# Kernel tuning notes

Measured on AMD Instinct MI355X. Metric: run time of the kernel, lower is better.

Reference implementation:

```python
import jax, jax.numpy as jnp
import numpy as np

EPS = 1e-6
NHEAD = 12

def _ln(x):
    m = jnp.mean(x, -1, keepdims=True)
    v = jnp.var(x, -1, keepdims=True)
    return (x - m) * jax.lax.rsqrt(v + EPS)

def _modulate(x, shift, scale):
    return x * (1 + scale[:, None, :]) + shift[:, None, :]

def _pos_embedding(idx, dim, max_len=2048):
    K = jnp.arange(dim // 2)
    ang = idx[..., None] * jnp.pi / (max_len ** (2.0 * K / dim))
    return jnp.concatenate([jnp.sin(ang), jnp.cos(ang)], axis=-1)

def _forward(x, W_xemb, b_xemb, ds_table, sg_table, Wqkv, bqkv, Wo, bo, W1, b1, W2, b2,
             Wada, bada, Wada_f, bada_f, W_out, dataset, spacegroup, mask):
    B, N, _ = x.shape
    D = W_xemb.shape[1]
    hd = D // NHEAD
    # conditioning vector: label embeddings (eval mode: no cfg dropout)
    c = ds_table[dataset] + sg_table[spacegroup]                 # [B, D]
    h = x @ W_xemb + b_xemb + _pos_embedding(jnp.arange(N), D)[None]  # [B, N, D]
    kmask = mask[:, None, None, :]                                # [B,1,1,N], True = padded key
    scale_qk = 1.0 / jnp.sqrt(jnp.asarray(hd, h.dtype))

    def block(h, p):
        Wqkv, bqkv, Wo, bo, W1, b1, W2, b2, Wada, bada = p
        mods = jax.nn.silu(c) @ Wada + bada                      # [B, 6D]
        sh_a, sc_a, g_a, sh_m, sc_m, g_m = jnp.split(mods, 6, axis=-1)
        xm = _modulate(_ln(h), sh_a, sc_a)
        qkv = (xm @ Wqkv + bqkv).reshape(B, N, 3, NHEAD, hd)
        q, k, v = qkv[:, :, 0], qkv[:, :, 1], qkv[:, :, 2]
        scores = jnp.einsum('bqhd,bkhd->bhqk', q, k) * scale_qk   # MATH-backend path: full [B,H,N,N]
        scores = jnp.where(kmask, -jnp.inf, scores)
        attn = jax.nn.softmax(scores, axis=-1)
        o = jnp.einsum('bhqk,bkhd->bqhd', attn, v).reshape(B, N, D)
        o = o @ Wo + bo
        h = h + g_a[:, None, :] * o
        y = _modulate(_ln(h), sh_m, sc_m)
        y = jax.nn.gelu(y @ W1 + b1, approximate=True) @ W2 + b2
        h = h + g_m[:, None, :] * y
        return h, None

    h, _ = jax.lax.scan(block, h, (Wqkv, bqkv, Wo, bo, W1, b1, W2, b2, Wada, bada))
    mods_f = jax.nn.silu(c) @ Wada_f + bada_f
    sh_f, sc_f = jnp.split(mods_f, 2, axis=-1)
    return _modulate(_ln(h), sh_f, sc_f) @ W_out                  # [B, N, 1] per-token energy


def setup_inputs() -> dict:
    B, N, D, L, DX, HID = 32, 512, 768, 12, 8, 3072
    keys = iter(jax.random.split(jax.random.key(0), 32))
    def w(shape, s=0.02):
        return jax.random.normal(next(keys), shape, jnp.float32) * s
    return dict(
        x=jax.random.normal(next(keys), (B, N, 2 * DX), jnp.float32),
        W_xemb=w((2 * DX, D)), b_xemb=jnp.zeros((D,), jnp.float32),
        ds_table=w((3, D)), sg_table=w((231, D)),
        Wqkv=w((L, D, 3 * D)), bqkv=jnp.zeros((L, 3 * D), jnp.float32),
        Wo=w((L, D, D)), bo=jnp.zeros((L, D), jnp.float32),
        W1=w((L, D, HID)), b1=jnp.zeros((L, HID), jnp.float32),
        W2=w((L, HID, D)), b2=jnp.zeros((L, D), jnp.float32),
        Wada=w((L, D, 6 * D)), bada=jnp.zeros((L, 6 * D), jnp.float32),
        Wada_f=w((D, 2 * D)), bada_f=jnp.zeros((2 * D,), jnp.float32),
        W_out=w((D, 1)),
        dataset=jax.random.randint(next(keys), (32,), 0, 2),
        spacegroup=jax.random.randint(next(keys), (32,), 0, 230),
        mask=jax.random.bernoulli(next(keys), 0.1, (32, 512)),
    )


def reference(x, W_xemb, b_xemb, ds_table, sg_table, Wqkv, bqkv, Wo, bo, W1, b1, W2, b2,
              Wada, bada, Wada_f, bada_f, W_out, dataset, spacegroup, mask):
    return _forward(x, W_xemb, b_xemb, ds_table, sg_table, Wqkv, bqkv, Wo, bo, W1, b1,
                    W2, b2, Wada, bada, Wada_f, bada_f, W_out, dataset, spacegroup, mask)
```

## Files before the change

### kernel.cpp

```cpp
#include <hip/hip_runtime.h>
#include <hip/hip_bf16.h>

#define B_   32
#define N_   512
#define D_   768
#define H_   12
#define HID_ 3072
#define L_   12
#define M_   (B_*N_)

typedef __attribute__((ext_vector_type(8))) short short8_t;
typedef __attribute__((ext_vector_type(4))) short short4_t;
typedef __attribute__((ext_vector_type(4))) float f32x4;
typedef __hip_bfloat16 bf16;

__device__ __forceinline__ void gll16(const void* g, void* l){
    __builtin_amdgcn_global_load_lds((const __attribute__((address_space(1))) void*)g,
                                     (__attribute__((address_space(3))) void*)l, 16, 0, 0);
}

__global__ __launch_bounds__(256) void embed_kernel(
    const float* __restrict__ x, const float* __restrict__ Wx,
    const float* __restrict__ bx, float* __restrict__ h)
{
    long idx = (long)blockIdx.x * 256 + threadIdx.x;
    int d = (int)(idx % 768);
    long m = idx / 768;
    int n = (int)(m % 512);
    float acc = bx[d];
    const float* xr = x + m * 16;
    #pragma unroll
    for (int k = 0; k < 16; ++k) acc = fmaf(xr[k], Wx[k*768 + d], acc);
    int K = (d < 384) ? d : d - 384;
    float ang = (float)n * 3.14159265358979323846f * expf(-(2.0f*(float)K/768.0f) * 7.624618986159398f);
    acc += (d < 384) ? sinf(ang) : cosf(ang);
    h[idx] = acc;
}

__global__ __launch_bounds__(256) void csilu_kernel(
    const float* __restrict__ ds_t, const float* __restrict__ sg_t,
    const int* __restrict__ dataset, const int* __restrict__ sg, float* __restrict__ out)
{
    int idx = blockIdx.x*256 + threadIdx.x;
    int b = idx / 768, d = idx % 768;
    float c = ds_t[dataset[b]*768 + d] + sg_t[sg[b]*768 + d];
    out[idx] = c / (1.0f + expf(-c));
}

__global__ __launch_bounds__(256) void mods_part_kernel(
    const float* __restrict__ csilu, const float* __restrict__ W,
    float* __restrict__ part, int Nd2, long wLayerStride)
{
    __shared__ float cs[16][96];
    int n2 = blockIdx.x*256 + threadIdx.x;
    int l = blockIdx.y, z = blockIdx.z;
    int kz = z >> 1, bg = z & 1;
    int L = gridDim.y;
    for (int t = threadIdx.x; t < 16*96; t += 256){
        int bb = t / 96, kk = t - bb*96;
        cs[bb][kk] = csilu[(bg*16 + bb)*768 + kz*96 + kk];
    }
    __syncthreads();
    const float2* Wl = (const float2*)(W + (long)l*wLayerStride);
    float2 acc[16];
    #pragma unroll
    for (int b=0;b<16;b++) acc[b] = make_float2(0.f, 0.f);
    for (int k=0;k<96;++k){
        float2 wv = Wl[(long)(kz*96 + k)*Nd2 + n2];
        #pragma unroll
        for (int b=0;b<16;b++){
            float c = cs[b][k];
            acc[b].x = fmaf(c, wv.x, acc[b].x);
            acc[b].y = fmaf(c, wv.y, acc[b].y);
        }
    }
    float2* pp = (float2*)part + ((long)(kz*L + l)*32 + bg*16)*Nd2 + n2;
    #pragma unroll
    for (int b=0;b<16;b++) pp[(long)b*Nd2] = acc[b];
}

__global__ __launch_bounds__(256) void mods_reduce_kernel(
    const float* __restrict__ part, const float* __restrict__ bias,
    float* __restrict__ out, int Nd, int L)
{
    long idx = (long)blockIdx.x*256 + threadIdx.x;
    int n = (int)(idx % Nd);
    long r = idx / Nd;
    int b = (int)(r & 31);
    int l = (int)(r >> 5);
    float s = bias[(long)l*Nd + n];
    #pragma unroll
    for (int z=0;z<8;z++) s += part[((long)(z*L + l)*32 + b)*Nd + n];
    out[idx] = s;
}

__global__ __launch_bounds__(256) void transpose4_kernel(
    const float* __restrict__ Wqkv, const float* __restrict__ Wo,
    const float* __restrict__ W1,  const float* __restrict__ W2,
    bf16* __restrict__ wqT, bf16* __restrict__ woT,
    bf16* __restrict__ w1T, bf16* __restrict__ w2T)
{
    __shared__ float t[32][33];
    int tt = blockIdx.x;
    const float* src; bf16* dst; int K, Nd, nx;
    if (tt < 1728){ src=Wqkv; dst=wqT; K=768; Nd=2304; nx=72; }
    else if (tt < 2304){ src=Wo; dst=woT; K=768; Nd=768; nx=24; tt -= 1728; }
    else if (tt < 4608){ src=W1; dst=w1T; K=768; Nd=3072; nx=96; tt -= 2304; }
    else { src=W2; dst=w2T; K=3072; Nd=768; nx=24; tt -= 4608; }
    int n0 = (tt % nx)*32, k0 = (tt / nx)*32;
    int tx = threadIdx.x & 31, ty = threadIdx.x >> 5;
    #pragma unroll
    for (int j=0;j<4;j++)
        t[ty + j*8][tx] = src[(long)(k0 + ty + j*8)*Nd + n0 + tx];
    __syncthreads();
    #pragma unroll
    for (int j=0;j<4;j++)
        dst[(long)(n0 + ty + j*8)*K + k0 + tx] = __float2bfloat16(t[tx][ty + j*8]);
}

__global__ __launch_bounds__(256) void ln_mod_kernel(
    const float* __restrict__ h, const float* __restrict__ shiftB,
    const float* __restrict__ scaleB, int modsStride, bf16* __restrict__ out)
{
    int wave = threadIdx.x >> 6, lane = threadIdx.x & 63;
    long row = (long)blockIdx.x*4 + wave;
    int b = (int)(row >> 9);
    const float4* xr = (const float4*)(h + row*768);
    float4 v[3];
    float s = 0.f, ss = 0.f;
    #pragma unroll
    for (int i=0;i<3;i++){
        v[i] = xr[lane + i*64];
        s  += v[i].x + v[i].y + v[i].z + v[i].w;
        ss += v[i].x*v[i].x + v[i].y*v[i].y + v[i].z*v[i].z + v[i].w*v[i].w;
    }
    #pragma unroll
    for (int o=1;o<64;o<<=1){ s += __shfl_xor(s,o,64); ss += __shfl_xor(ss,o,64); }
    float mean = s * (1.0f/768.0f);
    float var  = ss * (1.0f/768.0f) - mean*mean;
    float rstd = rsqrtf(var + 1e-6f);
    const float4* sh4 = (const float4*)(shiftB + (long)b*modsStride);
    const float4* sc4 = (const float4*)(scaleB + (long)b*modsStride);
    short4_t* orow = (short4_t*)(out + row*768);
    #pragma unroll
    for (int i=0;i<3;i++){
        float4 sh = sh4[lane + i*64];
        float4 sc = sc4[lane + i*64];
        float o0 = (v[i].x-mean)*rstd*(1.f+sc.x) + sh.x;
        float o1 = (v[i].y-mean)*rstd*(1.f+sc.y) + sh.y;
        float o2 = (v[i].z-mean)*rstd*(1.f+sc.z) + sh.z;
        float o3 = (v[i].w-mean)*rstd*(1.f+sc.w) + sh.w;
        bf16 b0 = __float2bfloat16(o0), b1 = __float2bfloat16(o1);
        bf16 b2 = __float2bfloat16(o2), b3 = __float2bfloat16(o3);
        short4_t pk;
        pk[0] = *(short*)&b0; pk[1] = *(short*)&b1;
        pk[2] = *(short*)&b2; pk[3] = *(short*)&b3;
        orow[lane + i*64] = pk;
    }
}

__device__ __forceinline__ float gelu_f(float x){
    float z2 = 1.5957691216057308f * x * (1.0f + 0.044715f*x*x);
    return x / (1.0f + __expf(-z2));
}

template<int MODE>
__global__ __launch_bounds__(256, 2) void gemm128_kernel(
    const bf16* __restrict__ A, const bf16* __restrict__ Bw,
    const float* __restrict__ bias, bf16* __restrict__ outBf,
    float* __restrict__ hres, const float* __restrict__ gate,
    int Nd, int Kd, int gateStride)
{
    __shared__ __align__(16) short lds[40960];
    int tid = threadIdx.x;
    int lane = tid & 63, wave = tid >> 6;
    int frow = lane & 15, g = lane >> 4;

    int nx = gridDim.x;
    int bid = blockIdx.y * nx + blockIdx.x;
    int xcd = bid & 7;
    int wq  = bid >> 3;
    int mt  = xcd * 16 + (wq & 15);
    int ct  = wq >> 4;
    int m0 = mt * 128, n0 = ct * 192;
    int wn = wave * 48;

    const short* Ag = (const short*)A;
    const short* Bg = (const short*)Bw;
    int r0 = tid >> 3, s0 = (tid & 7) ^ ((tid >> 3) & 7);
    const short* aSrc = Ag + (long)(m0 + r0)*Kd + s0*8;
    const short* bSrc = Bg + (long)(n0 + r0)*Kd + s0*8;
    long rj = (long)32*Kd;
    int wbase = wave*512;

    int aFrag = frow*64;
    int bFrag = (wn + frow)*64;
    int slotK0 = (g ^ (frow & 7))*8;
    int slotK1 = ((4+g) ^ (frow & 7))*8;

    f32x4 acc[8][3];
    #pragma unroll
    for (int i=0;i<8;i++)
        #pragma unroll
        for (int j=0;j<3;j++) acc[i][j] = (f32x4){0.f,0.f,0.f,0.f};

    int NT = Kd >> 6;

#define STAGE(kt, ps) { \
    int par_ = (kt)&1; \
    if ((ps)==0){ \
        short* d_ = &lds[par_*8192 + wbase]; \
        gll16(aSrc +        (long)(kt)*64, d_); \
        gll16(aSrc +   rj + (long)(kt)*64, d_ + 2048); \
        gll16(aSrc + 2*rj + (long)(kt)*64, d_ + 4096); \
        gll16(aSrc + 3*rj + (long)(kt)*64, d_ + 6144); \
    } else { \
        short* d_ = &lds[16384 + par_*12288 + wbase]; \
        gll16(bSrc +        (long)(kt)*64, d_); \
        gll16(bSrc +   rj + (long)(kt)*64, d_ + 2048); \
        gll16(bSrc + 2*rj + (long)(kt)*64, d_ + 4096); \
        gll16(bSrc + 3*rj + (long)(kt)*64, d_ + 6144); \
        gll16(bSrc + 4*rj + (long)(kt)*64, d_ + 8192); \
        gll16(bSrc + 5*rj + (long)(kt)*64, d_ + 10240); \
    } }

    STAGE(0,0); STAGE(0,1);

    for (int kt=0; kt<NT; ++kt){
        int pA  = (kt&1)*8192;
        int pBb = 16384 + (kt&1)*12288;
        bool pf = (kt+1 < NT);
        if (pf){
            STAGE(kt+1, 0);
            asm volatile("s_waitcnt vmcnt(4)" ::: "memory");
        } else {
            asm volatile("s_waitcnt vmcnt(0)" ::: "memory");
        }
        __builtin_amdgcn_s_barrier();
        __builtin_amdgcn_sched_barrier(0);
        short8_t af[8], bfr[3];
        #pragma unroll
        for (int i=0;i<8;i++) af[i]  = *(const short8_t*)&lds[pA + aFrag + i*1024 + slotK0];
        #pragma unroll
        for (int j=0;j<3;j++) bfr[j] = *(const short8_t*)&lds[pBb + bFrag + j*1024 + slotK0];
        if (pf) STAGE(kt+1, 1);
        __builtin_amdgcn_s_setprio(1);
        #pragma unroll
        for (int i=0;i<8;i++)
            #pragma unroll
            for (int j=0;j<3;j++)
                acc[i][j] = __builtin_amdgcn_mfma_f32_16x16x32_bf16(af[i], bfr[j], acc[i][j], 0, 0, 0);
        __builtin_amdgcn_s_setprio(0);
        #pragma unroll
        for (int i=0;i<8;i++) af[i]  = *(const short8_t*)&lds[pA + aFrag + i*1024 + slotK1];
        #pragma unroll
        for (int j=0;j<3;j++) bfr[j] = *(const short8_t*)&lds[pBb + bFrag + j*1024 + slotK1];
        __builtin_amdgcn_s_setprio(1);
        #pragma unroll
        for (int i=0;i<8;i++)
            #pragma unroll
            for (int j=0;j<3;j++)
                acc[i][j] = __builtin_amdgcn_mfma_f32_16x16x32_bf16(af[i], bfr[j], acc[i][j], 0, 0, 0);
        __builtin_amdgcn_s_setprio(0);
        __builtin_amdgcn_sched_barrier(0);
        __builtin_amdgcn_s_barrier();
        __builtin_amdgcn_sched_barrier(0);
    }
#undef STAGE

    int rbase = m0 + g*4;
    int cbase = n0 + wn + frow;
    float bv0 = bias[cbase], bv1 = bias[cbase+16], bv2 = bias[cbase+32];
    #pragma unroll
    for (int i=0;i<8;i++){
        #pragma unroll
        for (int r=0;r<4;r++){
            int row = rbase + i*16 + r;
            float v0 = acc[i][0][r] + bv0;
            float v1 = acc[i][1][r] + bv1;
            float v2 = acc[i][2][r] + bv2;
            if (MODE == 0){
                bf16* o_ = outBf + (long)row*Nd + cbase;
                o_[0]  = __float2bfloat16(v0);
                o_[16] = __float2bfloat16(v1);
                o_[32] = __float2bfloat16(v2);
            } else if (MODE == 1){
                bf16* o_ = outBf + (long)row*Nd + cbase;
                o_[0]  = __float2bfloat16(gelu_f(v0));
                o_[16] = __float2bfloat16(gelu_f(v1));
                o_[32] = __float2bfloat16(gelu_f(v2));
            } else {
                int bb = row >> 9;
                const float* gp = gate + (long)bb*gateStride + cbase;
                float* hp = hres + (long)row*768 + cbase;
                hp[0]  += gp[0]  * v0;
                hp[16] += gp[16] * v1;
                hp[32] += gp[32] * v2;
            }
        }
    }
}

template<int MODE>
__global__ __launch_bounds__(512, 2) void gemm256_kernel(
    const bf16* __restrict__ A, const bf16* __restrict__ Bw,
    const float* __restrict__ bias, bf16* __restrict__ outBf,
    float* __restrict__ hres, const float* __restrict__ gate,
    int Nd, int Kd, int gateStride)
{
    __shared__ __align__(16) short lds[65536];
    int tid = threadIdx.x;
    int lane = tid & 63, wave = tid >> 6;
    int frow = lane & 15, g = lane >> 4;
    int wm = wave >> 2, wn4 = wave & 3;

    int nwg = gridDim.x;
    int bid = blockIdx.x;
    int q8  = nwg >> 3;
    int wgid = (bid & 7) * q8 + (bid >> 3);
    int ntiles = Nd >> 8;
    int mt = wgid / ntiles, ct = wgid - mt*ntiles;
    int m0 = mt * 256, n0 = ct * 256;

    const short* Ag = (const short*)A;
    const short* Bg = (const short*)Bw;
    int r0 = tid >> 3;
    int s0 = (tid & 7) ^ (r0 & 7);
    const short* aSrc = Ag + (long)(m0 + r0)*Kd + s0*8;
    const short* bSrc = Bg + (long)(n0 + r0)*Kd + s0*8;
    long r64 = (long)64*Kd;
    int wb = wave*512;

    int aRd = wm*4096 + frow*64;
    int bRd = wn4*2048 + frow*64;
    int slotK0 = (g ^ (frow & 7))*8;
    int slotK1 = ((4+g) ^ (frow & 7))*8;

    f32x4 acc[8][4];
    #pragma unroll
    for (int i=0;i<8;i++)
        #pragma unroll
        for (int j=0;j<4;j++) acc[i][j] = (f32x4){0.f,0.f,0.f,0.f};

    short8_t af[4][2];
    short8_t bf[2][2];

    int NT = Kd >> 6;

#define STA(kt, h) { \
    short* d_ = &lds[((kt)&1)*16384 + (h)*8192 + wb]; \
    const short* s_ = aSrc + (long)(h)*2*r64 + (long)(kt)*64; \
    gll16(s_, d_); gll16(s_ + r64, d_ + 4096); }
#define STB(kt, h) { \
    short* d_ = &lds[32768 + ((kt)&1)*16384 + (h)*8192 + wb]; \
    const short* s_ = bSrc + (long)(h)*2*r64 + (long)(kt)*64; \
    gll16(s_, d_); gll16(s_ + r64, d_ + 4096); }

#define RDA(mh) { \
    int ba_ = pA + (mh)*8192 + aRd; \
    _Pragma("unroll") \
    for (int i=0;i<4;++i){ \
        af[i][0] = *(const short8_t*)&lds[ba_ + i*1024 + slotK0]; \
        af[i][1] = *(const short8_t*)&lds[ba_ + i*1024 + slotK1]; } }
#define RDB(nh) { \
    int bb_ = pB + (nh)*8192 + bRd; \
    _Pragma("unroll") \
    for (int j=0;j<2;++j){ \
        bf[j][0] = *(const short8_t*)&lds[bb_ + j*1024 + slotK0]; \
        bf[j][1] = *(const short8_t*)&lds[bb_ + j*1024 + slotK1]; } }

#define MFMA16(mh, nh) { \
    __builtin_amdgcn_s_setprio(1); \
    _Pragma("unroll") \
    for (int kh=0;kh<2;++kh) \
        _Pragma("unroll") \
        for (int i=0;i<4;++i) \
            _Pragma("unroll") \
            for (int j=0;j<2;++j) \
                acc[(mh)*4+i][(nh)*2+j] = __builtin_amdgcn_mfma_f32_16x16x32_bf16( \
                    af[i][kh], bf[j][kh], acc[(mh)*4+i][(nh)*2+j], 0, 0, 0); \
    __builtin_amdgcn_s_setprio(0); }

    STA(0,0); STB(0,0); STB(0,1); STA(0,1);
    asm volatile("s_waitcnt vmcnt(4)" ::: "memory");
    __builtin_amdgcn_s_barrier();
    __builtin_amdgcn_sched_barrier(0);

    for (int kt=0; kt<NT; ++kt){
        int pA = (kt&1)*16384;
        int pB = 32768 + (kt&1)*16384;
        bool pf = (kt+1 < NT);

        RDA(0); RDB(0);
        if (pf) STA(kt+1, 0);
        __builtin_amdgcn_sched_barrier(0);
        MFMA16(0, 0);
        if (pf) asm volatile("s_waitcnt vmcnt(4)" ::: "memory");
        else    asm volatile("s_waitcnt vmcnt(2)" ::: "memory");
        __builtin_amdgcn_s_barrier();
        __builtin_amdgcn_sched_barrier(0);

        RDB(1);
        if (pf) STB(kt+1, 0);
        __builtin_amdgcn_sched_barrier(0);
        MFMA16(0, 1);
        if (pf) asm volatile("s_waitcnt vmcnt(4)" ::: "memory");
        else    asm volatile("s_waitcnt vmcnt(0)" ::: "memory");
        __builtin_amdgcn_s_barrier();
        __builtin_amdgcn_sched_barrier(0);

        RDA(1);
        if (pf) STB(kt+1, 1);
        __builtin_amdgcn_sched_barrier(0);
        MFMA16(1, 1);
        __builtin_amdgcn_s_barrier();
        __builtin_amdgcn_sched_barrier(0);

        RDB(0);
        if (pf) STA(kt+1, 1);
        __builtin_amdgcn_sched_barrier(0);
        MFMA16(1, 0);
        if (pf) asm volatile("s_waitcnt vmcnt(4)" ::: "memory");
        __builtin_amdgcn_s_barrier();
        __builtin_amdgcn_sched_barrier(0);
    }
#undef STA
#undef STB
#undef RDA
#undef RDB
#undef MFMA16

    int rb = m0 + wm*64 + g*4;
    int cb = n0 + wn4*32 + frow;
    float bv0 = bias[cb], bv1 = bias[cb+16], bv2 = bias[cb+128], bv3 = bias[cb+144];
    #pragma unroll
    for (int mh=0; mh<2; ++mh){
        #pragma unroll
        for (int i=0;i<4;++i){
            #pragma unroll
            for (int r=0;r<4;++r){
                int row = rb + mh*128 + i*16 + r;
                float v0 = acc[mh*4+i][0][r] + bv0;
                float v1 = acc[mh*4+i][1][r] + bv1;
                float v2 = acc[mh*4+i][2][r] + bv2;
                float v3 = acc[mh*4+i][3][r] + bv3;
                if (MODE == 0){
                    bf16* o_ = outBf + (long)row*Nd + cb;
                    o_[0]   = __float2bfloat16(v0);
                    o_[16]  = __float2bfloat16(v1);
                    o_[128] = __float2bfloat16(v2);
                    o_[144] = __float2bfloat16(v3);
                } else if (MODE == 1){
                    bf16* o_ = outBf + (long)row*Nd + cb;
                    o_[0]   = __float2bfloat16(gelu_f(v0));
                    o_[16]  = __float2bfloat16(gelu_f(v1));
                    o_[128] = __float2bfloat16(gelu_f(v2));
                    o_[144] = __float2bfloat16(gelu_f(v3));
                } else {
                    int bb = row >> 9;
                    const float* gp = gate + (long)bb*gateStride + cb;
                    float* hp = hres + (long)row*768 + cb;
                    hp[0]   += gp[0]   * v0;
                    hp[16]  += gp[16]  * v1;
                    hp[128] += gp[128] * v2;
                    hp[144] += gp[144] * v3;
                }
            }
        }
    }
}

__global__ __launch_bounds__(256) void attn_mfma_kernel(
    const bf16* __restrict__ qkv, const int* __restrict__ mask, bf16* __restrict__ o)
{
    __shared__ __align__(16) short Ks[64][72];
    __shared__ __align__(16) short Vt[64][72];
    __shared__ __align__(16) short Ps[4][16][72];
    __shared__ float maskf[512];
    int tid = threadIdx.x, lane = tid & 63, wave = tid >> 6;
    int qt = blockIdx.x, hh = blockIdx.y, b = blockIdx.z;
    long base = (long)b * 512 * 2304;
    const short* qkvs = (const short*)qkv;

    maskf[tid]       = mask[b*512 + tid]       ? -1e30f : 0.0f;
    maskf[tid + 256] = mask[b*512 + tid + 256] ? -1e30f : 0.0f;

    int c = lane & 15, g = lane >> 4;
    int qrowA = qt*64 + wave*16 + c;
    const short* qptr = qkvs + base + (long)qrowA*2304 + hh*64 + g*8;
    short8_t qa0 = *(const short8_t*)qptr;
    short8_t qa1 = *(const short8_t*)(qptr + 32);

    f32x4 oacc[4];
    #pragma unroll
    for (int j=0;j<4;j++) oacc[j] = (f32x4){0.f,0.f,0.f,0.f};
    float m_r[4], l_r[4];
    #pragma unroll
    for (int r=0;r<4;r++){ m_r[r] = -50.0f; l_r[r] = 0.0f; }

    int kp = (tid & 31)*2, gv = tid >> 5;
    const short* kgbase = qkvs + base + 768  + hh*64;
    const short* vgbase = qkvs + base + 1536 + hh*64 + gv*8;

    for (int kt=0; kt<8; ++kt){
        __syncthreads();
        {
            int v0 = tid, v1 = tid + 256;
            int r0 = v0>>3, c0 = (v0&7)*8, r1 = v1>>3, c1 = (v1&7)*8;
            *(short8_t*)&Ks[r0][c0] = *(const short8_t*)(kgbase + (long)(kt*64 + r0)*2304 + c0);
            *(short8_t*)&Ks[r1][c1] = *(const short8_t*)(kgbase + (long)(kt*64 + r1)*2304 + c1);
            short8_t va = *(const short8_t*)(vgbase + (long)(kt*64 + kp    )*2304);
            short8_t vb = *(const short8_t*)(vgbase + (long)(kt*64 + kp + 1)*2304);
            #pragma unroll
            for (int e=0;e<8;e++){
                unsigned int pack = (unsigned int)(unsigned short)va[e]
                                  | ((unsigned int)(unsigned short)vb[e] << 16);
                *(unsigned int*)&Vt[gv*8 + e][kp] = pack;
            }
        }
        __syncthreads();
        f32x4 s[4];
        #pragma unroll
        for (int j=0;j<4;j++){
            short8_t kb0 = *(const short8_t*)&Ks[j*16 + c][g*8];
            short8_t kb1 = *(const short8_t*)&Ks[j*16 + c][g*8 + 32];
            f32x4 z = (f32x4){0.f,0.f,0.f,0.f};
            z = __builtin_amdgcn_mfma_f32_16x16x32_bf16(qa0, kb0, z, 0, 0, 0);
            z = __builtin_amdgcn_mfma_f32_16x16x32_bf16(qa1, kb1, z, 0, 0, 0);
            s[j] = z;
        }
        #pragma unroll
        for (int j=0;j<4;j++){
            float mbj = maskf[kt*64 + j*16 + c];
            #pragma unroll
            for (int r=0;r<4;r++) s[j][r] = s[j][r]*0.125f + mbj;
        }
        #pragma unroll
        for (int r=0;r<4;r++){
            float tm = fmaxf(fmaxf(s[0][r], s[1][r]), fmaxf(s[2][r], s[3][r]));
            #pragma unroll
            for (int o_=1;o_<16;o_<<=1) tm = fmaxf(tm, __shfl_xor(tm, o_, 64));
            float mn  = fmaxf(m_r[r], tm);
            float fac = __expf(m_r[r] - mn);
            m_r[r] = mn;
            float ls = l_r[r]*fac;
            #pragma unroll
            for (int j=0;j<4;j++){
                float p = __expf(s[j][r] - mn);
                s[j][r] = p;
                ls += p;
            }
            l_r[r] = ls;
            #pragma unroll
            for (int j=0;j<4;j++) oacc[j][r] *= fac;
        }
        #pragma unroll
        for (int j=0;j<4;j++)
            #pragma unroll
            for (int r=0;r<4;r++)
                *(bf16*)&Ps[wave][g*4 + r][j*16 + c] = __float2bfloat16(s[j][r]);
        short8_t pa0 = *(const short8_t*)&Ps[wave][c][g*8];
        short8_t pa1 = *(const short8_t*)&Ps[wave][c][g*8 + 32];
        #pragma unroll
        for (int j=0;j<4;j++){
            short8_t vb0 = *(const short8_t*)&Vt[j*16 + c][g*8];
            short8_t vb1 = *(const short8_t*)&Vt[j*16 + c][g*8 + 32];
            oacc[j] = __builtin_amdgcn_mfma_f32_16x16x32_bf16(pa0, vb0, oacc[j], 0, 0, 0);
            oacc[j] = __builtin_amdgcn_mfma_f32_16x16x32_bf16(pa1, vb1, oacc[j], 0, 0, 0);
        }
    }
    #pragma unroll
    for (int r=0;r<4;r++){
        float lt = l_r[r];
        #pragma unroll
        for (int o_=1;o_<16;o_<<=1) lt += __shfl_xor(lt, o_, 64);
        l_r[r] = 1.0f / lt;
    }
    int qrowC = qt*64 + wave*16 + g*4;
    bf16* orow = o + ((long)b*512 + qrowC)*768 + hh*64;
    #pragma unroll
    for (int r=0;r<4;r++)
        #pragma unroll
        for (int j=0;j<4;j++)
            orow[(long)r*768 + j*16 + c] = __float2bfloat16(oacc[j][r] * l_r[r]);
}

__global__ __launch_bounds__(256) void outdot_kernel(
    const bf16* __restrict__ xm, const float* __restrict__ Wout, float* __restrict__ out)
{
    int tid=threadIdx.x, lane=tid&63, wave=tid>>6;
    long row = (long)blockIdx.x*4 + wave;
    const bf16* xr = xm + row*768;
    float acc = 0.f;
    #pragma unroll
    for (int i=0;i<12;i++){ int d = lane + i*64; acc = fmaf(__bfloat162float(xr[d]), Wout[d], acc); }
    #pragma unroll
    for (int o_=1;o_<64;o_<<=1) acc += __shfl_xor(acc, o_, 64);
    if (lane==0) out[row] = acc;
}

extern "C" void kernel_launch(void* const* d_in, const int* in_sizes, int n_in,
                              void* d_out, int out_size, void* d_ws, size_t ws_size,
                              hipStream_t stream)
{
    const float* x      = (const float*)d_in[0];
    const float* W_xemb = (const float*)d_in[1];
    const float* b_xemb = (const float*)d_in[2];
    const float* ds_t   = (const float*)d_in[3];
    const float* sg_t   = (const float*)d_in[4];
    const float* Wqkv   = (const float*)d_in[5];
    const float* bqkv   = (const float*)d_in[6];
    const float* Wo     = (const float*)d_in[7];
    const float* bo     = (const float*)d_in[8];
    const float* W1     = (const float*)d_in[9];
    const float* b1     = (const float*)d_in[10];
    const float* W2     = (const float*)d_in[11];
    const float* b2     = (const float*)d_in[12];
    const float* Wada   = (const float*)d_in[13];
    const float* bada   = (const float*)d_in[14];
    const float* Wada_f = (const float*)d_in[15];
    const float* bada_f = (const float*)d_in[16];
    const float* W_out  = (const float*)d_in[17];
    const int* dataset  = (const int*)d_in[18];
    const int* sgroup   = (const int*)d_in[19];
    const int* mask     = (const int*)d_in[20];
    float* out = (float*)d_out;

    char* ws = (char*)d_ws;
    size_t off = 0;
    auto alloc = [&](size_t bytes)->void*{
        void* p = ws + off; off += (bytes + 255) & ~(size_t)255; return p; };
    float* h     = (float*)alloc((size_t)M_*768*4);
    float* csilu = (float*)alloc((size_t)32*768*4);
    float* modsA = (float*)alloc((size_t)12*32*4608*4);
    float* modsF = (float*)alloc((size_t)32*1536*4);
    bf16*  xm    = (bf16*) alloc((size_t)M_*768*2);
    bf16*  wbuf  = (bf16*) alloc((size_t)7077888*2);
    bf16*  big   = (bf16*) alloc((size_t)M_*3072*2);
    bf16* qkvb = big;
    bf16* y1   = big;
    float* partA = (float*)big;
    float* partF = partA + (size_t)8*12*32*4608;
    bf16* wqT = wbuf;
    bf16* woT = wqT + 2304*768;
    bf16* w1T = woT + 768*768;
    bf16* w2T = w1T + 3072*768;

    embed_kernel<<<49152, 256, 0, stream>>>(x, W_xemb, b_xemb, h);
    csilu_kernel<<<96, 256, 0, stream>>>(ds_t, sg_t, dataset, sgroup, csilu);
    mods_part_kernel<<<dim3(9,12,16), 256, 0, stream>>>(csilu, Wada, partA, 2304, (long)768*4608);
    mods_reduce_kernel<<<6912, 256, 0, stream>>>(partA, bada, modsA, 4608, 12);
    mods_part_kernel<<<dim3(3,1,16), 256, 0, stream>>>(csilu, Wada_f, partF, 768, 0);
    mods_reduce_kernel<<<192, 256, 0, stream>>>(partF, bada_f, modsF, 1536, 1);

    for (int l=0; l<12; ++l){
        const float* modsL = modsA + (long)l*32*4608;
        transpose4_kernel<<<6912, 256, 0, stream>>>(
            Wqkv + (long)l*768*2304, Wo + (long)l*768*768,
            W1 + (long)l*768*3072,  W2 + (long)l*3072*768,
            wqT, woT, w1T, w2T);

        ln_mod_kernel<<<4096, 256, 0, stream>>>(h, modsL + 0*768, modsL + 1*768, 4608, xm);
        gemm128_kernel<0><<<dim3(12, 128), 256, 0, stream>>>(xm, wqT, bqkv + l*2304, qkvb,
                                                             nullptr, nullptr, 2304, 768, 0);
        attn_mfma_kernel<<<dim3(8, 12, 32), 256, 0, stream>>>(qkvb, mask, xm);
        gemm128_kernel<2><<<dim3(4, 128), 256, 0, stream>>>(xm, woT, bo + l*768, nullptr,
                                                            h, modsL + 2*768, 768, 768, 4608);
        ln_mod_kernel<<<4096, 256, 0, stream>>>(h, modsL + 3*768, modsL + 4*768, 4608, xm);
        gemm256_kernel<1><<<768, 512, 0, stream>>>(xm, w1T, b1 + l*3072, y1,
                                                   nullptr, nullptr, 3072, 768, 0);
        gemm128_kernel<2><<<dim3(4, 128), 256, 0, stream>>>(y1, w2T, b2 + l*768, nullptr,
                                                            h, modsL + 5*768, 768, 3072, 4608);
    }
    ln_mod_kernel<<<4096, 256, 0, stream>>>(h, modsF + 0, modsF + 768, 1536, xm);
    outdot_kernel<<<4096, 256, 0, stream>>>(xm, W_out, out);
}
```

Before: 4.818 ms.

## Deepen GEMM256 prefetch pipeline, batch gemm128 LDS reads, precompute positional table

```diff
diff --git a/kernel.cpp b/kernel.cpp
--- a/kernel.cpp
+++ b/kernel.cpp
@@ -19,21 +19,28 @@
                                      (__attribute__((address_space(3))) void*)l, 16, 0, 0);
 }
 
+__global__ __launch_bounds__(256) void pos_kernel(float* __restrict__ ptab)
+{
+    int idx = blockIdx.x*256 + threadIdx.x;
+    int d = idx % 768, n = idx / 768;
+    int K = (d < 384) ? d : d - 384;
+    float ang = (float)n * 3.14159265358979323846f * expf(-(2.0f*(float)K/768.0f) * 7.624618986159398f);
+    ptab[idx] = (d < 384) ? sinf(ang) : cosf(ang);
+}
+
 __global__ __launch_bounds__(256) void embed_kernel(
     const float* __restrict__ x, const float* __restrict__ Wx,
-    const float* __restrict__ bx, float* __restrict__ h)
+    const float* __restrict__ bx, const float* __restrict__ ptab,
+    float* __restrict__ h)
 {
     long idx = (long)blockIdx.x * 256 + threadIdx.x;
     int d = (int)(idx % 768);
     long m = idx / 768;
     int n = (int)(m % 512);
-    float acc = bx[d];
+    float acc = bx[d] + ptab[n*768 + d];
     const float* xr = x + m * 16;
     #pragma unroll
     for (int k = 0; k < 16; ++k) acc = fmaf(xr[k], Wx[k*768 + d], acc);
-    int K = (d < 384) ? d : d - 384;
-    float ang = (float)n * 3.14159265358979323846f * expf(-(2.0f*(float)K/768.0f) * 7.624618986159398f);
-    acc += (d < 384) ? sinf(ang) : cosf(ang);
     h[idx] = acc;
 }
 
@@ -238,29 +245,29 @@
         }
         __builtin_amdgcn_s_barrier();
         __builtin_amdgcn_sched_barrier(0);
-        short8_t af[8], bfr[3];
-        #pragma unroll
-        for (int i=0;i<8;i++) af[i]  = *(const short8_t*)&lds[pA + aFrag + i*1024 + slotK0];
-        #pragma unroll
-        for (int j=0;j<3;j++) bfr[j] = *(const short8_t*)&lds[pBb + bFrag + j*1024 + slotK0];
         if (pf) STAGE(kt+1, 1);
+        short8_t af0[8], af1[8], bf0[3], bf1[3];
+        #pragma unroll
+        for (int i=0;i<8;i++){
+            af0[i] = *(const short8_t*)&lds[pA + aFrag + i*1024 + slotK0];
+            af1[i] = *(const short8_t*)&lds[pA + aFrag + i*1024 + slotK1];
+        }
+        #pragma unroll
+        for (int j=0;j<3;j++){
+            bf0[j] = *(const short8_t*)&lds[pBb + bFrag + j*1024 + slotK0];
+            bf1[j] = *(const short8_t*)&lds[pBb + bFrag + j*1024 + slotK1];
+        }
         __builtin_amdgcn_s_setprio(1);
         #pragma unroll
         for (int i=0;i<8;i++)
             #pragma unroll
             for (int j=0;j<3;j++)
-                acc[i][j] = __builtin_amdgcn_mfma_f32_16x16x32_bf16(af[i], bfr[j], acc[i][j], 0, 0, 0);
-        __builtin_amdgcn_s_setprio(0);
-        #pragma unroll
-        for (int i=0;i<8;i++) af[i]  = *(const short8_t*)&lds[pA + aFrag + i*1024 + slotK1];
-        #pragma unroll
-        for (int j=0;j<3;j++) bfr[j] = *(const short8_t*)&lds[pBb + bFrag + j*1024 + slotK1];
-        __builtin_amdgcn_s_setprio(1);
+                acc[i][j] = __builtin_amdgcn_mfma_f32_16x16x32_bf16(af0[i], bf0[j], acc[i][j], 0, 0, 0);
         #pragma unroll
         for (int i=0;i<8;i++)
             #pragma unroll
             for (int j=0;j<3;j++)
-                acc[i][j] = __builtin_amdgcn_mfma_f32_16x16x32_bf16(af[i], bfr[j], acc[i][j], 0, 0, 0);
+                acc[i][j] = __builtin_amdgcn_mfma_f32_16x16x32_bf16(af1[i], bf1[j], acc[i][j], 0, 0, 0);
         __builtin_amdgcn_s_setprio(0);
         __builtin_amdgcn_sched_barrier(0);
         __builtin_amdgcn_s_barrier();
@@ -302,11 +309,10 @@
 }
 
 template<int MODE>
-__global__ __launch_bounds__(512, 2) void gemm256_kernel(
+__global__ __launch_bounds__(512, 2) void gemm256v2_kernel(
     const bf16* __restrict__ A, const bf16* __restrict__ Bw,
     const float* __restrict__ bias, bf16* __restrict__ outBf,
-    float* __restrict__ hres, const float* __restrict__ gate,
-    int Nd, int Kd, int gateStride)
+    int Nd, int Kd)
 {
     __shared__ __align__(16) short lds[65536];
     int tid = threadIdx.x;
@@ -333,8 +339,8 @@
 
     int aRd = wm*4096 + frow*64;
     int bRd = wn4*2048 + frow*64;
-    int slotK0 = (g ^ (frow & 7))*8;
-    int slotK1 = ((4+g) ^ (frow & 7))*8;
+    int sk0 = (g ^ (frow & 7))*8;
+    int sk1 = ((4+g) ^ (frow & 7))*8;
 
     f32x4 acc[8][4];
     #pragma unroll
@@ -342,34 +348,18 @@
         #pragma unroll
         for (int j=0;j<4;j++) acc[i][j] = (f32x4){0.f,0.f,0.f,0.f};
 
-    short8_t af[4][2];
-    short8_t bf[2][2];
-
     int NT = Kd >> 6;
 
-#define STA(kt, h) { \
-    short* d_ = &lds[((kt)&1)*16384 + (h)*8192 + wb]; \
-    const short* s_ = aSrc + (long)(h)*2*r64 + (long)(kt)*64; \
+#define STA(t, h) { \
+    short* d_ = &lds[((t)&1)*16384 + (h)*8192 + wb]; \
+    const short* s_ = aSrc + (long)(h)*2*r64 + (long)(t)*64; \
     gll16(s_, d_); gll16(s_ + r64, d_ + 4096); }
-#define STB(kt, h) { \
-    short* d_ = &lds[32768 + ((kt)&1)*16384 + (h)*8192 + wb]; \
-    const short* s_ = bSrc + (long)(h)*2*r64 + (long)(kt)*64; \
+#define STB(t, h) { \
+    short* d_ = &lds[32768 + ((t)&1)*16384 + (h)*8192 + wb]; \
+    const short* s_ = bSrc + (long)(h)*2*r64 + (long)(t)*64; \
     gll16(s_, d_); gll16(s_ + r64, d_ + 4096); }
 
-#define RDA(mh) { \
-    int ba_ = pA + (mh)*8192 + aRd; \
-    _Pragma("unroll") \
-    for (int i=0;i<4;++i){ \
-        af[i][0] = *(const short8_t*)&lds[ba_ + i*1024 + slotK0]; \
-        af[i][1] = *(const short8_t*)&lds[ba_ + i*1024 + slotK1]; } }
-#define RDB(nh) { \
-    int bb_ = pB + (nh)*8192 + bRd; \
-    _Pragma("unroll") \
-    for (int j=0;j<2;++j){ \
-        bf[j][0] = *(const short8_t*)&lds[bb_ + j*1024 + slotK0]; \
-        bf[j][1] = *(const short8_t*)&lds[bb_ + j*1024 + slotK1]; } }
-
-#define MFMA16(mh, nh) { \
+#define MFMA_Q(mh, nh, AF, BF) { \
     __builtin_amdgcn_s_setprio(1); \
     _Pragma("unroll") \
     for (int kh=0;kh<2;++kh) \
@@ -378,57 +368,75 @@
             _Pragma("unroll") \
             for (int j=0;j<2;++j) \
                 acc[(mh)*4+i][(nh)*2+j] = __builtin_amdgcn_mfma_f32_16x16x32_bf16( \
-                    af[i][kh], bf[j][kh], acc[(mh)*4+i][(nh)*2+j], 0, 0, 0); \
+                    AF[i][kh], BF[j][kh], acc[(mh)*4+i][(nh)*2+j], 0, 0, 0); \
     __builtin_amdgcn_s_setprio(0); }
 
     STA(0,0); STB(0,0); STB(0,1); STA(0,1);
-    asm volatile("s_waitcnt vmcnt(4)" ::: "memory");
+    STA(1,0); STB(1,0); STB(1,1);
+    asm volatile("s_waitcnt vmcnt(6)" ::: "memory");
     __builtin_amdgcn_s_barrier();
     __builtin_amdgcn_sched_barrier(0);
 
     for (int kt=0; kt<NT; ++kt){
         int pA = (kt&1)*16384;
         int pB = 32768 + (kt&1)*16384;
-        bool pf = (kt+1 < NT);
-
-        RDA(0); RDB(0);
-        if (pf) STA(kt+1, 0);
-        __builtin_amdgcn_sched_barrier(0);
-        MFMA16(0, 0);
-        if (pf) asm volatile("s_waitcnt vmcnt(4)" ::: "memory");
-        else    asm volatile("s_waitcnt vmcnt(2)" ::: "memory");
-        __builtin_amdgcn_s_barrier();
-        __builtin_amdgcn_sched_barrier(0);
-
-        RDB(1);
-        if (pf) STB(kt+1, 0);
-        __builtin_amdgcn_sched_barrier(0);
-        MFMA16(0, 1);
-        if (pf) asm volatile("s_waitcnt vmcnt(4)" ::: "memory");
-        else    asm volatile("s_waitcnt vmcnt(0)" ::: "memory");
-        __builtin_amdgcn_s_barrier();
-        __builtin_amdgcn_sched_barrier(0);
-
-        RDA(1);
-        if (pf) STB(kt+1, 1);
-        __builtin_amdgcn_sched_barrier(0);
-        MFMA16(1, 1);
-        __builtin_amdgcn_s_barrier();
-        __builtin_amdgcn_sched_barrier(0);
-
-        RDB(0);
-        if (pf) STA(kt+1, 1);
-        __builtin_amdgcn_sched_barrier(0);
-        MFMA16(1, 0);
-        if (pf) asm volatile("s_waitcnt vmcnt(4)" ::: "memory");
+        short8_t af0[4][2], af1[4][2], bf0[2][2], bf1[2][2];
+
+        #pragma unroll
+        for (int i=0;i<4;++i){
+            af0[i][0] = *(const short8_t*)&lds[pA + aRd + i*1024 + sk0];
+            af0[i][1] = *(const short8_t*)&lds[pA + aRd + i*1024 + sk1];
+        }
+        #pragma unroll
+        for (int j=0;j<2;++j){
+            bf0[j][0] = *(const short8_t*)&lds[pB + bRd + j*1024 + sk0];
+            bf0[j][1] = *(const short8_t*)&lds[pB + bRd + j*1024 + sk1];
+        }
+        if (kt+1 < NT) STA(kt+1, 1);
+        asm volatile("s_waitcnt lgkmcnt(8)" ::: "memory");
+        __builtin_amdgcn_s_barrier();
+        asm volatile("s_waitcnt lgkmcnt(0)" ::: "memory");
+        __builtin_amdgcn_sched_barrier(0);
+        MFMA_Q(0, 0, af0, bf0);
+        __builtin_amdgcn_s_barrier();
+
+        #pragma unroll
+        for (int i=0;i<4;++i){
+            af1[i][0] = *(const short8_t*)&lds[pA + 8192 + aRd + i*1024 + sk0];
+            af1[i][1] = *(const short8_t*)&lds[pA + 8192 + aRd + i*1024 + sk1];
+        }
+        if (kt+2 < NT) STA(kt+2, 0);
+        __builtin_amdgcn_s_barrier();
+        asm volatile("s_waitcnt lgkmcnt(0)" ::: "memory");
+        __builtin_amdgcn_sched_barrier(0);
+        MFMA_Q(1, 0, af1, bf0);
+        __builtin_amdgcn_s_barrier();
+
+        #pragma unroll
+        for (int j=0;j<2;++j){
+            bf1[j][0] = *(const short8_t*)&lds[pB + 8192 + bRd + j*1024 + sk0];
+            bf1[j][1] = *(const short8_t*)&lds[pB + 8192 + bRd + j*1024 + sk1];
+        }
+        if (kt+2 < NT) STB(kt+2, 0);
+        __builtin_amdgcn_s_barrier();
+        asm volatile("s_waitcnt lgkmcnt(0)" ::: "memory");
+        __builtin_amdgcn_sched_barrier(0);
+        MFMA_Q(1, 1, af1, bf1);
+        __builtin_amdgcn_s_barrier();
+
+        if (kt+2 < NT) STB(kt+2, 1);
+        __builtin_amdgcn_s_barrier();
+        __builtin_amdgcn_sched_barrier(0);
+        MFMA_Q(0, 1, af0, bf1);
+        __builtin_amdgcn_sched_barrier(0);
+        if (kt < NT-2) { asm volatile("s_waitcnt vmcnt(6)" ::: "memory"); }
+        else           { asm volatile("s_waitcnt vmcnt(0)" ::: "memory"); }
         __builtin_amdgcn_s_barrier();
         __builtin_amdgcn_sched_barrier(0);
     }
 #undef STA
 #undef STB
-#undef RDA
-#undef RDB
-#undef MFMA16
+#undef MFMA_Q
 
     int rb = m0 + wm*64 + g*4;
     int cb = n0 + wn4*32 + frow;
@@ -444,27 +452,14 @@
                 float v1 = acc[mh*4+i][1][r] + bv1;
                 float v2 = acc[mh*4+i][2][r] + bv2;
                 float v3 = acc[mh*4+i][3][r] + bv3;
-                if (MODE == 0){
-                    bf16* o_ = outBf + (long)row*Nd + cb;
-                    o_[0]   = __float2bfloat16(v0);
-                    o_[16]  = __float2bfloat16(v1);
-                    o_[128] = __float2bfloat16(v2);
-                    o_[144] = __float2bfloat16(v3);
-                } else if (MODE == 1){
-                    bf16* o_ = outBf + (long)row*Nd + cb;
-                    o_[0]   = __float2bfloat16(gelu_f(v0));
-                    o_[16]  = __float2bfloat16(gelu_f(v1));
-                    o_[128] = __float2bfloat16(gelu_f(v2));
-                    o_[144] = __float2bfloat16(gelu_f(v3));
-                } else {
-                    int bb = row >> 9;
-                    const float* gp = gate + (long)bb*gateStride + cb;
-                    float* hp = hres + (long)row*768 + cb;
-                    hp[0]   += gp[0]   * v0;
-                    hp[16]  += gp[16]  * v1;
-                    hp[128] += gp[128] * v2;
-                    hp[144] += gp[144] * v3;
+                bf16* o_ = outBf + (long)row*Nd + cb;
+                if (MODE == 1){
+                    v0 = gelu_f(v0); v1 = gelu_f(v1); v2 = gelu_f(v2); v3 = gelu_f(v3);
                 }
+                o_[0]   = __float2bfloat16(v0);
+                o_[16]  = __float2bfloat16(v1);
+                o_[128] = __float2bfloat16(v2);
+                o_[144] = __float2bfloat16(v3);
             }
         }
     }
@@ -634,6 +629,7 @@
     float* csilu = (float*)alloc((size_t)32*768*4);
     float* modsA = (float*)alloc((size_t)12*32*4608*4);
     float* modsF = (float*)alloc((size_t)32*1536*4);
+    float* ptab  = (float*)alloc((size_t)512*768*4);
     bf16*  xm    = (bf16*) alloc((size_t)M_*768*2);
     bf16*  wbuf  = (bf16*) alloc((size_t)7077888*2);
     bf16*  big   = (bf16*) alloc((size_t)M_*3072*2);
@@ -646,7 +642,8 @@
     bf16* w1T = woT + 768*768;
     bf16* w2T = w1T + 3072*768;
 
-    embed_kernel<<<49152, 256, 0, stream>>>(x, W_xemb, b_xemb, h);
+    pos_kernel<<<1536, 256, 0, stream>>>(ptab);
+    embed_kernel<<<49152, 256, 0, stream>>>(x, W_xemb, b_xemb, ptab, h);
     csilu_kernel<<<96, 256, 0, stream>>>(ds_t, sg_t, dataset, sgroup, csilu);
     mods_part_kernel<<<dim3(9,12,16), 256, 0, stream>>>(csilu, Wada, partA, 2304, (long)768*4608);
     mods_reduce_kernel<<<6912, 256, 0, stream>>>(partA, bada, modsA, 4608, 12);
@@ -667,8 +664,7 @@
         gemm128_kernel<2><<<dim3(4, 128), 256, 0, stream>>>(xm, woT, bo + l*768, nullptr,
                                                             h, modsL + 2*768, 768, 768, 4608);
         ln_mod_kernel<<<4096, 256, 0, stream>>>(h, modsL + 3*768, modsL + 4*768, 4608, xm);
-        gemm256_kernel<1><<<768, 512, 0, stream>>>(xm, w1T, b1 + l*3072, y1,
-                                                   nullptr, nullptr, 3072, 768, 0);
+        gemm256v2_kernel<1><<<768, 512, 0, stream>>>(xm, w1T, b1 + l*3072, y1, 3072, 768);
         gemm128_kernel<2><<<dim3(4, 128), 256, 0, stream>>>(y1, w2T, b2 + l*768, nullptr,
                                                             h, modsL + 5*768, 768, 3072, 4608);
     }
```

Result: no change. 4.837 ms (+0.4%).
